# Kernel optimization log

Measured on AMD Instinct MI355X. Metric: run time of the kernel, lower is better.

Reference implementation:

```python
import jax, jax.numpy as jnp
import numpy as np

B, T = 4, 96
IN_DIM, OUT_DIM, HID = 16, 16, 16
REL = 2 * IN_DIM  # until=True -> cat(interval max, interval min)
BIG = 1e9


def interval_pooling(a, reduction):
    # a: [b, t, t, d]; out[b,i,j] = reduce over a[b,k,l] for all i<=k<=l<=j
    t = a.shape[1]
    mask = jnp.triu(jnp.ones((t, t), dtype=bool))[None, :, :, None]
    if reduction == 'max':
        fill, cum = -BIG, jax.lax.cummax
    else:
        fill, cum = BIG, jax.lax.cummin
    x = jnp.where(mask, a, fill)
    x = cum(x, axis=1, reverse=True)  # over start k >= i
    x = cum(x, axis=2)                # over end   l <= j
    return jnp.where(mask, x, 0.0)


def dp_step(f, r, W, b):
    # linear_input[b,i,k,j] = cat(f[b,i,k], r[b,k,j]); MLPLogic = Linear+sigmoid;
    # transition_pooling_2d1d = max over k (dim 2). Split W so the wide cubic
    # concat is never materialized (same math as cat + matmul).
    df = f.shape[-1]
    Wf, Wr = W[:df], W[df:]
    ft = jnp.einsum('bikd,dh->bikh', f, Wf)[:, :, :, None, :]  # [b,i,k,1,h]
    rt = jnp.einsum('bkjd,dh->bkjh', r, Wr)[:, None, :, :, :]  # [b,1,k,j,h]
    g = jax.nn.sigmoid(ft + rt + b)  # [b, t+1, t+1, t+1, h] cubic intermediate
    return jnp.max(g, axis=2)        # pool over transition point k


def setup_inputs() -> dict:
    key = jax.random.key(0)
    ks = jax.random.split(key, 7)
    a = jax.random.normal(ks[0], (B, T, T, IN_DIM), jnp.float32)
    W0 = 0.1 * jax.random.normal(ks[1], (REL + REL, HID), jnp.float32)
    b0 = 0.1 * jax.random.normal(ks[2], (HID,), jnp.float32)
    W1 = 0.1 * jax.random.normal(ks[3], (HID + REL + REL, HID), jnp.float32)
    b1 = 0.1 * jax.random.normal(ks[4], (HID,), jnp.float32)
    W2 = 0.1 * jax.random.normal(ks[5], (HID + REL, OUT_DIM), jnp.float32)
    b2 = 0.1 * jax.random.normal(ks[6], (OUT_DIM,), jnp.float32)
    return {'a': a, 'W0': W0, 'b0': b0, 'W1': W1, 'b1': b1, 'W2': W2, 'b2': b2}


def reference(a, W0, b0, W1, b1, W2, b2):
    bsz, t = a.shape[0], a.shape[1]
    r = jnp.concatenate([interval_pooling(a, 'max'),
                         interval_pooling(a, 'min')], axis=-1)  # [b,t,t,2*in]
    f = jnp.zeros((bsz, t + 1, t + 1, r.shape[-1]), a.dtype)
    f = f.at[:, :-1, 1:].set(r)  # pad to boundary indexing [b,t+1,t+1,rel]
    r = f
    # step 0
    f = dp_step(f, r, W0, b0)
    f = jnp.concatenate([f, r], axis=-1)  # residual_input
    # step 1
    f = dp_step(f, r, W1, b1)
    f = jnp.concatenate([f, r], axis=-1)
    # final MLPLogic
    f = jax.nn.sigmoid(f @ W2 + b2)
    return f[:, :-1, 1:]
```

## Files before the change

kernel.cpp:

```cpp
#include <hip/hip_runtime.h>
#include <hip/hip_bf16.h>

#define RS   100
#define PLS  9700
#define NP   9409

#define OFF_R   0
#define OFF_A   (OFF_R  + 4*32*PLS)
#define OFF_Bm  (OFF_A  + 4*16*PLS)
#define OFF_F1  (OFF_Bm + 4*16*PLS)
#define OFF_F2  (OFF_F1 + 4*16*PLS)

__device__ __forceinline__ float sigm(float x) { return 1.0f / (1.0f + __expf(-x)); }

__global__ __launch_bounds__(128) void pool_kernel(const float* __restrict__ a, float* __restrict__ R) {
    __shared__ float s[96][97];
    const int tid = threadIdx.x;
    const int b  = blockIdx.x >> 5;
    const int ch = blockIdx.x & 31;
    const int d  = ch & 15;
    const bool isMin = (ch >= 16);

    for (int idx = tid; idx < 96 * 96; idx += 128) {
        int i = idx / 96, j = idx - i * 96;
        float v = a[((size_t)(b * 96 + i) * 96 + j) * 16 + d];
        if (isMin) v = -v;
        s[i][j] = (j >= i) ? v : -1e30f;
    }
    __syncthreads();
    if (tid < 96) {
        int j = tid; float run = -1e30f;
#pragma unroll 4
        for (int i = 95; i >= 0; --i) { run = fmaxf(run, s[i][j]); s[i][j] = run; }
    }
    __syncthreads();
    if (tid < 96) {
        int i = tid; float run = -1e30f;
#pragma unroll 4
        for (int j = 0; j < 96; ++j) { run = fmaxf(run, s[i][j]); s[i][j] = run; }
    }
    __syncthreads();
    float* Rp = R + (size_t)blockIdx.x * PLS;
    for (int idx = tid; idx < 97 * 97; idx += 128) {
        int x = idx / 97, y = idx - x * 97;
        float v = 0.f;
        if (x <= 95 && y >= 1 && x <= y - 1) { v = s[x][y - 1]; if (isMin) v = -v; }
        Rp[x * RS + y] = v;
    }
}

__global__ __launch_bounds__(256) void proj0_kernel(const float* __restrict__ R, const float* __restrict__ W,
                                                    float* __restrict__ A, float* __restrict__ B) {
    const int bh = blockIdx.y, b = bh >> 4, h = bh & 15;
    const int p = blockIdx.x * 256 + threadIdx.x;
    if (p >= NP) return;
    const int x = p / 97, y = p - x * 97;
    const int off = x * RS + y;
    const float* Rb = R + (size_t)b * 32 * PLS + off;
    float accA = 0.f, accB = 0.f;
#pragma unroll
    for (int d = 0; d < 32; ++d) {
        float rv = Rb[(size_t)d * PLS];
        accA += rv * W[d * 16 + h];
        accB += rv * W[(32 + d) * 16 + h];
    }
    A[(size_t)bh * PLS + off] = accA;
    B[(size_t)bh * PLS + off] = accB;
}

__global__ __launch_bounds__(256) void proj1_kernel(const float* __restrict__ R, const float* __restrict__ F1,
                                                    const float* __restrict__ W,
                                                    float* __restrict__ A, float* __restrict__ B) {
    const int bh = blockIdx.y, b = bh >> 4, h = bh & 15;
    const int p = blockIdx.x * 256 + threadIdx.x;
    if (p >= NP) return;
    const int x = p / 97, y = p - x * 97;
    const int off = x * RS + y;
    const float* Rb = R  + (size_t)b * 32 * PLS + off;
    const float* Fb = F1 + (size_t)b * 16 * PLS + off;
    float accA = 0.f, accB = 0.f;
#pragma unroll
    for (int c = 0; c < 16; ++c) accA += Fb[(size_t)c * PLS] * W[c * 16 + h];
#pragma unroll
    for (int d = 0; d < 32; ++d) {
        float rv = Rb[(size_t)d * PLS];
        accA += rv * W[(16 + d) * 16 + h];
        accB += rv * W[(48 + d) * 16 + h];
    }
    A[(size_t)bh * PLS + off] = accA;
    B[(size_t)bh * PLS + off] = accB;
}

__global__ __launch_bounds__(256) void maxplus_kernel(const float* __restrict__ A, const float* __restrict__ Bm,
                                                      const float* __restrict__ bias, float* __restrict__ F) {
    __shared__ alignas(16) float As[97][36];
    __shared__ alignas(16) float Bs[97][36];
    const int tid = threadIdx.x;
    const int bh = blockIdx.y;
    const int h  = bh & 15;
    const int i0 = (blockIdx.x & 3) * 32;
    const int j0 = (blockIdx.x >> 2) * 32;
    const float* Ab = A  + (size_t)bh * PLS;
    const float* Bb = Bm + (size_t)bh * PLS;

    for (int idx = tid; idx < 32 * 97; idx += 256) {
        int r = idx / 97, k = idx - r * 97;
        int ii = i0 + r;
        As[k][r] = (ii < 97) ? Ab[ii * RS + k] : -1e30f;
    }
    for (int idx = tid; idx < 97 * 32; idx += 256) {
        int k = idx >> 5, c = idx & 31;
        int jj = j0 + c;
        Bs[k][c] = (jj < 97) ? Bb[k * RS + jj] : -1e30f;
    }
    __syncthreads();

    const int ty = tid >> 4, tx = tid & 15;
    float a00 = -1e30f, a01 = -1e30f, a10 = -1e30f, a11 = -1e30f;

#pragma unroll 4
    for (int k = 0; k < 97; ++k) {
        const float2 a2 = *reinterpret_cast<const float2*>(&As[k][ty * 2]);
        const float2 b2 = *reinterpret_cast<const float2*>(&Bs[k][tx * 2]);
        a00 = fmaxf(a00, a2.x + b2.x);
        a01 = fmaxf(a01, a2.x + b2.y);
        a10 = fmaxf(a10, a2.y + b2.x);
        a11 = fmaxf(a11, a2.y + b2.y);
    }

    const float bb = bias[h];
    float* Fb = F + (size_t)bh * PLS;
    const int col0 = j0 + tx * 2;
    const int row0 = i0 + ty * 2;
    float v[2][2] = {{a00, a01}, {a10, a11}};
#pragma unroll
    for (int r = 0; r < 2; ++r) {
        const int row = row0 + r;
        if (row > 96) continue;
        if (col0 + 1 <= 96) {
            float2 o;
            o.x = sigm(v[r][0] + bb);
            o.y = sigm(v[r][1] + bb);
            *reinterpret_cast<float2*>(&Fb[row * RS + col0]) = o;
        } else if (col0 <= 96) {
            Fb[row * RS + col0] = sigm(v[r][0] + bb);
        }
    }
}

__global__ __launch_bounds__(256) void final_kernel(const float* __restrict__ R, const float* __restrict__ F2,
                                                    const float* __restrict__ W, const float* __restrict__ bias,
                                                    float* __restrict__ out) {
    const int p = blockIdx.x * 256 + threadIdx.x;
    if (p >= 4 * 96 * 96) return;
    const int oj = p % 96;
    const int t1 = p / 96;
    const int i  = t1 % 96;
    const int b  = t1 / 96;
    const int off = i * RS + (oj + 1);
    const float* Fb = F2 + (size_t)b * 16 * PLS + off;
    const float* Rb = R  + (size_t)b * 32 * PLS + off;
    float acc[16];
#pragma unroll
    for (int o = 0; o < 16; ++o) acc[o] = bias[o];
#pragma unroll
    for (int c = 0; c < 16; ++c) {
        const float fv = Fb[(size_t)c * PLS];
#pragma unroll
        for (int o = 0; o < 16; ++o) acc[o] += fv * W[c * 16 + o];
    }
#pragma unroll
    for (int d = 0; d < 32; ++d) {
        const float rv = Rb[(size_t)d * PLS];
#pragma unroll
        for (int o = 0; o < 16; ++o) acc[o] += rv * W[(16 + d) * 16 + o];
    }
    float4* dst = reinterpret_cast<float4*>(out + (size_t)p * 16);
#pragma unroll
    for (int q = 0; q < 4; ++q) {
        float4 v;
        v.x = sigm(acc[q * 4 + 0]);
        v.y = sigm(acc[q * 4 + 1]);
        v.z = sigm(acc[q * 4 + 2]);
        v.w = sigm(acc[q * 4 + 3]);
        dst[q] = v;
    }
}

extern "C" void kernel_launch(void* const* d_in, const int* in_sizes, int n_in,
                              void* d_out, int out_size, void* d_ws, size_t ws_size,
                              hipStream_t stream) {
    const float* a  = (const float*)d_in[0];
    const float* W0 = (const float*)d_in[1];
    const float* b0 = (const float*)d_in[2];
    const float* W1 = (const float*)d_in[3];
    const float* b1 = (const float*)d_in[4];
    const float* W2 = (const float*)d_in[5];
    const float* b2 = (const float*)d_in[6];
    float* ws = (float*)d_ws;
    float* out = (float*)d_out;

    hipLaunchKernelGGL(pool_kernel, dim3(128), dim3(128), 0, stream, a, ws + OFF_R);
    hipLaunchKernelGGL(proj0_kernel, dim3(37, 64), dim3(256), 0, stream,
                       ws + OFF_R, W0, ws + OFF_A, ws + OFF_Bm);
    hipLaunchKernelGGL(maxplus_kernel, dim3(16, 64), dim3(256), 0, stream,
                       ws + OFF_A, ws + OFF_Bm, b0, ws + OFF_F1);
    hipLaunchKernelGGL(proj1_kernel, dim3(37, 64), dim3(256), 0, stream,
                       ws + OFF_R, ws + OFF_F1, W1, ws + OFF_A, ws + OFF_Bm);
    hipLaunchKernelGGL(maxplus_kernel, dim3(16, 64), dim3(256), 0, stream,
                       ws + OFF_A, ws + OFF_Bm, b1, ws + OFF_F2);
    hipLaunchKernelGGL(final_kernel, dim3(144), dim3(256), 0, stream,
                       ws + OFF_R, ws + OFF_F2, W2, b2, out);
}
```

Before: 160.0 us.

## Fuse all stages into one cooperative persistent kernel with grid syncs

Replaces the six-kernel launch chain with a single cooperative kernel that runs pooling, both projections, both max-plus steps and the final MLP as grid-stride phases separated by grid.sync. The goal is to remove per-launch overhead and inter-kernel gaps. Interval pooling is rewritten as two global passes through a temporary buffer instead of a shared-memory tile. The max-plus tiles are split into two k-chunks so shared memory fits several blocks per CU. Grid barriers and scattered global access in the pooling phase may cost more than the launch overhead they remove. The old multi-kernel path is kept as a fallback.

```diff
diff --git a/kernel.cpp b/kernel.cpp
--- a/kernel.cpp
+++ b/kernel.cpp
@@ -1,5 +1,8 @@
 #include <hip/hip_runtime.h>
 #include <hip/hip_bf16.h>
+#include <hip/hip_cooperative_groups.h>
+
+namespace cg = cooperative_groups;
 
 #define RS   100
 #define PLS  9700
@@ -10,8 +13,248 @@
 #define OFF_Bm  (OFF_A  + 4*16*PLS)
 #define OFF_F1  (OFF_Bm + 4*16*PLS)
 #define OFF_F2  (OFF_F1 + 4*16*PLS)
+#define OFF_T   (OFF_F2 + 4*16*PLS)
+
+#define MAXPLUS_TILES 1024
 
 __device__ __forceinline__ float sigm(float x) { return 1.0f / (1.0f + __expf(-x)); }
+
+__global__ __launch_bounds__(256, 4) void fused_all(
+        const float* __restrict__ a,
+        const float* __restrict__ W0, const float* __restrict__ b0,
+        const float* __restrict__ W1, const float* __restrict__ b1,
+        const float* __restrict__ W2, const float* __restrict__ b2,
+        float* __restrict__ ws, float* __restrict__ out) {
+    cg::grid_group grid = cg::this_grid();
+    __shared__ float As[49 * 36];
+    __shared__ float Bs[49 * 36];
+    const int tid = threadIdx.x;
+    const int gsz = gridDim.x * 256;
+    const int gtid = blockIdx.x * 256 + tid;
+
+    float* R  = ws + OFF_R;
+    float* A  = ws + OFF_A;
+    float* Bm = ws + OFF_Bm;
+    float* F1 = ws + OFF_F1;
+    float* F2 = ws + OFF_F2;
+    float* T  = ws + OFF_T;
+
+    for (int p = gtid; p < 128 * 96; p += gsz) {
+        const int plane = p / 96, j = p - (p / 96) * 96;
+        const int b = plane >> 5, ch = plane & 31, d = ch & 15;
+        const bool isMin = (ch >= 16);
+        const float* ab = a + ((size_t)(b * 96) * 96 + j) * 16 + d;
+        float* Tp = T + (size_t)plane * 9216 + j;
+        float run = -1e30f;
+        for (int i = 95; i >= 0; --i) {
+            float v = ab[(size_t)i * 96 * 16];
+            if (isMin) v = -v;
+            run = fmaxf(run, (j >= i) ? v : -1e30f);
+            Tp[i * 96] = run;
+        }
+    }
+    grid.sync();
+
+    for (int p = gtid; p < 128 * 97; p += gsz) {
+        const int plane = p / 97, x = p - (p / 97) * 97;
+        const int ch = plane & 31;
+        const bool isMin = (ch >= 16);
+        float* Rrow = R + (size_t)plane * PLS + x * RS;
+        Rrow[0] = 0.f;
+        if (x == 96) {
+            for (int y = 1; y < 97; ++y) Rrow[y] = 0.f;
+        } else {
+            const float* Tp = T + (size_t)plane * 9216 + x * 96;
+            float run = -1e30f;
+            for (int j = 0; j < 96; ++j) {
+                run = fmaxf(run, Tp[j]);
+                float v = 0.f;
+                if (j >= x) v = isMin ? -run : run;
+                Rrow[j + 1] = v;
+            }
+        }
+    }
+    grid.sync();
+
+    for (int p = gtid; p < 64 * NP; p += gsz) {
+        const int bh = p / NP, idx = p - bh * NP;
+        const int b = bh >> 4, h = bh & 15;
+        const int x = idx / 97, y = idx - (idx / 97) * 97;
+        const int off = x * RS + y;
+        const float* Rb = R + (size_t)b * 32 * PLS + off;
+        float accA = 0.f, accB = 0.f;
+#pragma unroll
+        for (int d = 0; d < 32; ++d) {
+            float rv = Rb[(size_t)d * PLS];
+            accA += rv * W0[d * 16 + h];
+            accB += rv * W0[(32 + d) * 16 + h];
+        }
+        A[(size_t)bh * PLS + off]  = accA;
+        Bm[(size_t)bh * PLS + off] = accB;
+    }
+    grid.sync();
+
+    for (int t = blockIdx.x; t < MAXPLUS_TILES; t += gridDim.x) {
+        const int bh = t >> 4, tt = t & 15;
+        const int h = bh & 15;
+        const int i0 = (tt & 3) * 32, j0 = (tt >> 2) * 32;
+        const float* Ab = A  + (size_t)bh * PLS;
+        const float* Bb = Bm + (size_t)bh * PLS;
+        const int ty = tid >> 4, tx = tid & 15;
+        float a00 = -1e30f, a01 = -1e30f, a10 = -1e30f, a11 = -1e30f;
+        int kbase = 0;
+#pragma unroll
+        for (int chunk = 0; chunk < 2; ++chunk) {
+            const int CH = chunk == 0 ? 49 : 48;
+            __syncthreads();
+            for (int idx = tid; idx < CH * 32; idx += 256) {
+                int r = idx / CH, kk = idx - r * CH;
+                int ii = i0 + r;
+                As[kk * 36 + r] = (ii < 97) ? Ab[ii * RS + kbase + kk] : -1e30f;
+            }
+            for (int idx = tid; idx < CH * 32; idx += 256) {
+                int kk = idx >> 5, c = idx & 31;
+                int jj = j0 + c;
+                Bs[kk * 36 + c] = (jj < 97) ? Bb[(kbase + kk) * RS + jj] : -1e30f;
+            }
+            __syncthreads();
+            for (int kk = 0; kk < CH; ++kk) {
+                const float2 a2 = *reinterpret_cast<const float2*>(&As[kk * 36 + ty * 2]);
+                const float2 b2v = *reinterpret_cast<const float2*>(&Bs[kk * 36 + tx * 2]);
+                a00 = fmaxf(a00, a2.x + b2v.x);
+                a01 = fmaxf(a01, a2.x + b2v.y);
+                a10 = fmaxf(a10, a2.y + b2v.x);
+                a11 = fmaxf(a11, a2.y + b2v.y);
+            }
+            kbase += CH;
+        }
+        const float bb = b0[h];
+        float* Fb = F1 + (size_t)bh * PLS;
+        const int col0 = j0 + tx * 2, row0 = i0 + ty * 2;
+        float v[2][2] = {{a00, a01}, {a10, a11}};
+#pragma unroll
+        for (int r = 0; r < 2; ++r) {
+            const int row = row0 + r;
+            if (row > 96) continue;
+            if (col0 + 1 <= 96) {
+                float2 o; o.x = sigm(v[r][0] + bb); o.y = sigm(v[r][1] + bb);
+                *reinterpret_cast<float2*>(&Fb[row * RS + col0]) = o;
+            } else if (col0 <= 96) {
+                Fb[row * RS + col0] = sigm(v[r][0] + bb);
+            }
+        }
+    }
+    grid.sync();
+
+    for (int p = gtid; p < 64 * NP; p += gsz) {
+        const int bh = p / NP, idx = p - bh * NP;
+        const int b = bh >> 4, h = bh & 15;
+        const int x = idx / 97, y = idx - (idx / 97) * 97;
+        const int off = x * RS + y;
+        const float* Rb = R  + (size_t)b * 32 * PLS + off;
+        const float* Fb = F1 + (size_t)b * 16 * PLS + off;
+        float accA = 0.f, accB = 0.f;
+#pragma unroll
+        for (int c = 0; c < 16; ++c) accA += Fb[(size_t)c * PLS] * W1[c * 16 + h];
+#pragma unroll
+        for (int d = 0; d < 32; ++d) {
+            float rv = Rb[(size_t)d * PLS];
+            accA += rv * W1[(16 + d) * 16 + h];
+            accB += rv * W1[(48 + d) * 16 + h];
+        }
+        A[(size_t)bh * PLS + off]  = accA;
+        Bm[(size_t)bh * PLS + off] = accB;
+    }
+    grid.sync();
+
+    for (int t = blockIdx.x; t < MAXPLUS_TILES; t += gridDim.x) {
+        const int bh = t >> 4, tt = t & 15;
+        const int h = bh & 15;
+        const int i0 = (tt & 3) * 32, j0 = (tt >> 2) * 32;
+        const float* Ab = A  + (size_t)bh * PLS;
+        const float* Bb = Bm + (size_t)bh * PLS;
+        const int ty = tid >> 4, tx = tid & 15;
+        float a00 = -1e30f, a01 = -1e30f, a10 = -1e30f, a11 = -1e30f;
+        int kbase = 0;
+#pragma unroll
+        for (int chunk = 0; chunk < 2; ++chunk) {
+            const int CH = chunk == 0 ? 49 : 48;
+            __syncthreads();
+            for (int idx = tid; idx < CH * 32; idx += 256) {
+                int r = idx / CH, kk = idx - r * CH;
+                int ii = i0 + r;
+                As[kk * 36 + r] = (ii < 97) ? Ab[ii * RS + kbase + kk] : -1e30f;
+            }
+            for (int idx = tid; idx < CH * 32; idx += 256) {
+                int kk = idx >> 5, c = idx & 31;
+                int jj = j0 + c;
+                Bs[kk * 36 + c] = (jj < 97) ? Bb[(kbase + kk) * RS + jj] : -1e30f;
+            }
+            __syncthreads();
+            for (int kk = 0; kk < CH; ++kk) {
+                const float2 a2 = *reinterpret_cast<const float2*>(&As[kk * 36 + ty * 2]);
+                const float2 b2v = *reinterpret_cast<const float2*>(&Bs[kk * 36 + tx * 2]);
+                a00 = fmaxf(a00, a2.x + b2v.x);
+                a01 = fmaxf(a01, a2.x + b2v.y);
+                a10 = fmaxf(a10, a2.y + b2v.x);
+                a11 = fmaxf(a11, a2.y + b2v.y);
+            }
+            kbase += CH;
+        }
+        const float bb = b1[h];
+        float* Fb = F2 + (size_t)bh * PLS;
+        const int col0 = j0 + tx * 2, row0 = i0 + ty * 2;
+        float v[2][2] = {{a00, a01}, {a10, a11}};
+#pragma unroll
+        for (int r = 0; r < 2; ++r) {
+            const int row = row0 + r;
+            if (row > 96) continue;
+            if (col0 + 1 <= 96) {
+                float2 o; o.x = sigm(v[r][0] + bb); o.y = sigm(v[r][1] + bb);
+                *reinterpret_cast<float2*>(&Fb[row * RS + col0]) = o;
+            } else if (col0 <= 96) {
+                Fb[row * RS + col0] = sigm(v[r][0] + bb);
+            }
+        }
+    }
+    grid.sync();
+
+    for (int p = gtid; p < 4 * 96 * 96; p += gsz) {
+        const int oj = p % 96;
+        const int t1 = p / 96;
+        const int i  = t1 % 96;
+        const int b  = t1 / 96;
+        const int off = i * RS + (oj + 1);
+        const float* Fb = F2 + (size_t)b * 16 * PLS + off;
+        const float* Rb = R  + (size_t)b * 32 * PLS + off;
+        float acc[16];
+#pragma unroll
+        for (int o = 0; o < 16; ++o) acc[o] = b2[o];
+#pragma unroll
+        for (int c = 0; c < 16; ++c) {
+            const float fv = Fb[(size_t)c * PLS];
+#pragma unroll
+            for (int o = 0; o < 16; ++o) acc[o] += fv * W2[c * 16 + o];
+        }
+#pragma unroll
+        for (int d = 0; d < 32; ++d) {
+            const float rv = Rb[(size_t)d * PLS];
+#pragma unroll
+            for (int o = 0; o < 16; ++o) acc[o] += rv * W2[(16 + d) * 16 + o];
+        }
+        float4* dst = reinterpret_cast<float4*>(out + (size_t)p * 16);
+#pragma unroll
+        for (int q = 0; q < 4; ++q) {
+            float4 v;
+            v.x = sigm(acc[q * 4 + 0]);
+            v.y = sigm(acc[q * 4 + 1]);
+            v.z = sigm(acc[q * 4 + 2]);
+            v.w = sigm(acc[q * 4 + 3]);
+            dst[q] = v;
+        }
+    }
+}
+
 
 __global__ __launch_bounds__(128) void pool_kernel(const float* __restrict__ a, float* __restrict__ R) {
     __shared__ float s[96][97];
@@ -20,7 +263,6 @@
     const int ch = blockIdx.x & 31;
     const int d  = ch & 15;
     const bool isMin = (ch >= 16);
-
     for (int idx = tid; idx < 96 * 96; idx += 128) {
         int i = idx / 96, j = idx - i * 96;
         float v = a[((size_t)(b * 96 + i) * 96 + j) * 16 + d];
@@ -30,13 +272,11 @@
     __syncthreads();
     if (tid < 96) {
         int j = tid; float run = -1e30f;
-#pragma unroll 4
         for (int i = 95; i >= 0; --i) { run = fmaxf(run, s[i][j]); s[i][j] = run; }
     }
     __syncthreads();
     if (tid < 96) {
         int i = tid; float run = -1e30f;
-#pragma unroll 4
         for (int j = 0; j < 96; ++j) { run = fmaxf(run, s[i][j]); s[i][j] = run; }
     }
     __syncthreads();
@@ -102,7 +342,6 @@
     const int j0 = (blockIdx.x >> 2) * 32;
     const float* Ab = A  + (size_t)bh * PLS;
     const float* Bb = Bm + (size_t)bh * PLS;
-
     for (int idx = tid; idx < 32 * 97; idx += 256) {
         int r = idx / 97, k = idx - r * 97;
         int ii = i0 + r;
@@ -114,10 +353,8 @@
         Bs[k][c] = (jj < 97) ? Bb[k * RS + jj] : -1e30f;
     }
     __syncthreads();
-
     const int ty = tid >> 4, tx = tid & 15;
     float a00 = -1e30f, a01 = -1e30f, a10 = -1e30f, a11 = -1e30f;
-
 #pragma unroll 4
     for (int k = 0; k < 97; ++k) {
         const float2 a2 = *reinterpret_cast<const float2*>(&As[k][ty * 2]);
@@ -127,7 +364,6 @@
         a10 = fmaxf(a10, a2.y + b2.x);
         a11 = fmaxf(a11, a2.y + b2.y);
     }
-
     const float bb = bias[h];
     float* Fb = F + (size_t)bh * PLS;
     const int col0 = j0 + tx * 2;
@@ -187,19 +423,10 @@
     }
 }
 
-extern "C" void kernel_launch(void* const* d_in, const int* in_sizes, int n_in,
-                              void* d_out, int out_size, void* d_ws, size_t ws_size,
-                              hipStream_t stream) {
-    const float* a  = (const float*)d_in[0];
-    const float* W0 = (const float*)d_in[1];
-    const float* b0 = (const float*)d_in[2];
-    const float* W1 = (const float*)d_in[3];
-    const float* b1 = (const float*)d_in[4];
-    const float* W2 = (const float*)d_in[5];
-    const float* b2 = (const float*)d_in[6];
-    float* ws = (float*)d_ws;
-    float* out = (float*)d_out;
-
+static void launch_fallback(const float* a, const float* W0, const float* b0,
+                            const float* W1, const float* b1,
+                            const float* W2, const float* b2,
+                            float* ws, float* out, hipStream_t stream) {
     hipLaunchKernelGGL(pool_kernel, dim3(128), dim3(128), 0, stream, a, ws + OFF_R);
     hipLaunchKernelGGL(proj0_kernel, dim3(37, 64), dim3(256), 0, stream,
                        ws + OFF_R, W0, ws + OFF_A, ws + OFF_Bm);
@@ -212,3 +439,33 @@
     hipLaunchKernelGGL(final_kernel, dim3(144), dim3(256), 0, stream,
                        ws + OFF_R, ws + OFF_F2, W2, b2, out);
 }
+
+extern "C" void kernel_launch(void* const* d_in, const int* in_sizes, int n_in,
+                              void* d_out, int out_size, void* d_ws, size_t ws_size,
+                              hipStream_t stream) {
+    const float* a  = (const float*)d_in[0];
+    const float* W0 = (const float*)d_in[1];
+    const float* b0 = (const float*)d_in[2];
+    const float* W1 = (const float*)d_in[3];
+    const float* b1 = (const float*)d_in[4];
+    const float* W2 = (const float*)d_in[5];
+    const float* b2 = (const float*)d_in[6];
+    float* ws  = (float*)d_ws;
+    float* out = (float*)d_out;
+
+    int perCU = 0, numCU = 0;
+    hipError_t e1 = hipOccupancyMaxActiveBlocksPerMultiprocessor(&perCU, (const void*)fused_all, 256, 0);
+    hipError_t e2 = hipDeviceGetAttribute(&numCU, hipDeviceAttributeMultiprocessorCount, 0);
+
+    bool coop_ok = (e1 == hipSuccess && e2 == hipSuccess && perCU >= 1 && numCU >= 1);
+    if (coop_ok) {
+        long long maxBlk = (long long)perCU * numCU;
+        int gridBlocks = (int)(maxBlk < MAXPLUS_TILES ? maxBlk : MAXPLUS_TILES);
+        void* args[] = {(void*)&a, (void*)&W0, (void*)&b0, (void*)&W1, (void*)&b1,
+                        (void*)&W2, (void*)&b2, (void*)&ws, (void*)&out};
+        hipError_t el = hipLaunchCooperativeKernel((const void*)fused_all, dim3(gridBlocks),
+                                                   dim3(256), args, 0, stream);
+        if (el == hipSuccess) return;
+    }
+    launch_fallback(a, W0, b0, W1, b1, W2, b2, ws, out, stream);
+}
```

New measurement: 584.6 us. 265% more time.
